# Kernel tuning notes

Hardware: AMD Instinct MI355X
Metric: run time of the kernel (lower is better)

The kernel has to match this reference:

```python
import jax, jax.numpy as jnp
import numpy as np

LAMBDA_REG = 0.1


def setup_inputs() -> dict:
    key = jax.random.key(0)
    k1, k2, k3, k4 = jax.random.split(key, 4)
    B, C, D = 4096, 10000, 128
    logits = jax.random.normal(k1, (B, C), dtype=jnp.float32)
    margins = jax.random.uniform(k2, (C,), dtype=jnp.float32)
    weights = jax.random.normal(k3, (C, D), dtype=jnp.float32)
    label = jax.random.randint(k4, (B,), 0, C, dtype=jnp.int64)
    return {"logits": logits, "margins": margins, "weights": weights, "label": label}


def reference(logits, margins, weights, label):
    B, C = logits.shape
    rows = jnp.arange(B)

    # F.cross_entropy(logits, label): mean NLL of log_softmax
    logp = jax.nn.log_softmax(logits, axis=-1)
    ce = -jnp.mean(logp[rows, label])

    # margin regularization
    margin_reg = LAMBDA_REG * jnp.mean(margins)

    # intra-class angular loss
    theta_yi = jnp.arccos(jnp.clip(logits[rows, label] / LAMBDA_REG, -1.0, 1.0))
    intra_loss = jnp.mean(theta_yi) / jnp.pi

    # inter-class loss: sum_i sum_{j != y_i} acos(clamp(w_{y_i} . w_j))
    # Vectorized replacement of the O(B*C) Python double loop:
    wy = weights[label]                       # (B, D) gather of ground-truth class rows
    S = jnp.einsum('bd,cd->bc', wy, weights)  # (B, C) pairwise dot products
    A = jnp.arccos(jnp.clip(S, -1.0, 1.0))    # (B, C) angles
    inter_sum = jnp.sum(A) - jnp.sum(A[rows, label])  # exclude j == y_i terms
    inter_loss = inter_sum / (B * (C - 1) * jnp.pi)

    return ce + margin_reg + intra_loss + inter_loss
```

## Files before the change

kernel.cpp:

```cpp
#include <hip/hip_runtime.h>
#include <stdint.h>
#include <math.h>

typedef __attribute__((ext_vector_type(8))) __bf16 bf16x8;
typedef __attribute__((ext_vector_type(4))) float floatx4;

constexpr int kB = 4096;
constexpr int kC = 10000;
constexpr int kD = 128;
constexpr int kNT = 79;
constexpr int kMT = 32;
constexpr int kBricksB = kNT * 32;
constexpr int kBricksA = kMT * 32;
constexpr int kPrepBlocks = (kBricksB + kBricksA) / 4;
constexpr float kPI = 3.14159265358979323846f;
constexpr float kLambda = 0.1f;
constexpr float kInvInter = (float)(1.0 / (4096.0 * 9999.0 * 3.141592653589793));

constexpr int kMegaBlocks = kB + kNT * kMT;
constexpr int kPerXcd = kMegaBlocks / 8;

constexpr size_t kBrickBytes = (size_t)(kBricksB + kBricksA) * 1024;
constexpr int kPartMargin = 0;
constexpr int kPartCE = 1;
constexpr int kPartInter = 1 + kB;
constexpr int kNumPart = 1 + kB + kNT * kMT;

__device__ __forceinline__ float fast_acos(float x) {
    float t = fabsf(x);
    float s = sqrtf(fmaxf(1.0f - t, 0.0f));
    float p = fmaf(fmaf(fmaf(-0.0187293f, t, 0.0742610f), t, -0.2121144f),
                   t, 1.5707288f);
    float r = s * p;
    return x < 0.0f ? kPI - r : r;
}

__device__ __forceinline__ uint16_t f2bf(float f) {
    union { float f; uint32_t u; } c; c.f = f;
    uint32_t u = c.u;
    uint32_t r = (u + 0x7FFFu + ((u >> 16) & 1u)) >> 16;
    return (uint16_t)r;
}

__global__ __launch_bounds__(256) void prep_kernel(
    const float* __restrict__ W, const float* __restrict__ margins,
    const int* __restrict__ label, uint16_t* __restrict__ wsB,
    uint16_t* __restrict__ wsA, float* __restrict__ part) {
    int blk = blockIdx.x;
    if (blk < kPrepBlocks) {
        int brick = blk * 4 + (threadIdx.x >> 6);
        int lane = threadIdx.x & 63;
        bool isA = brick >= kBricksB;
        int b2 = isA ? (brick - kBricksB) : brick;
        int kk = b2 & 3;
        int rb = (b2 >> 2) & 7;
        int tile = b2 >> 5;
        int row = tile * 128 + rb * 16 + (lane & 15);
        int k = kk * 32 + (lane >> 4) * 8;
        float v[8];
        if (isA) {
            int r = label[row];
            const float* src = W + (size_t)r * kD + k;
            #pragma unroll
            for (int j = 0; j < 8; ++j) v[j] = src[j];
        } else if (row < kC) {
            const float* src = W + (size_t)row * kD + k;
            #pragma unroll
            for (int j = 0; j < 8; ++j) v[j] = src[j];
        } else {
            #pragma unroll
            for (int j = 0; j < 8; ++j) v[j] = 0.0f;
        }
        uint4 pk;
        pk.x = (uint32_t)f2bf(v[0]) | ((uint32_t)f2bf(v[1]) << 16);
        pk.y = (uint32_t)f2bf(v[2]) | ((uint32_t)f2bf(v[3]) << 16);
        pk.z = (uint32_t)f2bf(v[4]) | ((uint32_t)f2bf(v[5]) << 16);
        pk.w = (uint32_t)f2bf(v[6]) | ((uint32_t)f2bf(v[7]) << 16);
        uint4* dst = (uint4*)(isA ? wsA : wsB);
        dst[(size_t)b2 * 64 + lane] = pk;
    } else {
        float s = 0.0f;
        for (int i = threadIdx.x; i < kC; i += 256) s += margins[i];
        for (int off = 32; off; off >>= 1) s += __shfl_down(s, off);
        __shared__ float p[4];
        if ((threadIdx.x & 63) == 0) p[threadIdx.x >> 6] = s;
        __syncthreads();
        if (threadIdx.x == 0)
            part[kPartMargin] = (p[0] + p[1] + p[2] + p[3]) * (kLambda / (float)kC);
    }
}

__global__ __launch_bounds__(256) void mega_kernel(
    const float* __restrict__ logits, const int* __restrict__ label,
    const uint16_t* __restrict__ wsA, const uint16_t* __restrict__ wsB,
    float* __restrict__ part) {
    int b = blockIdx.x;
    int x = b & 7;
    int q = b >> 3;
    int nce = (x < 6) ? 508 : 524;
    int cestart = (x < 6) ? 508 * x : 3048 + 524 * (x - 6);
    int cb = (q * nce) / kPerXcd;
    bool isce = ((q + 1) * nce) / kPerXcd > cb;
    int tid = threadIdx.x;

    if (isce) {
        int row = cestart + cb;
        const float* lp = logits + (size_t)row * kC;
        const floatx4* lp4 = (const floatx4*)lp;
        float s0 = 0.0f, s1 = 0.0f, s2 = 0.0f, s3 = 0.0f;
        floatx4 v[5];
        #pragma unroll
        for (int k = 0; k < 5; ++k)
            v[k] = __builtin_nontemporal_load(&lp4[tid + k * 256]);
        #pragma unroll
        for (int k = 0; k < 5; ++k) {
            s0 += __expf(v[k].x); s1 += __expf(v[k].y);
            s2 += __expf(v[k].z); s3 += __expf(v[k].w);
        }
        #pragma unroll
        for (int k = 0; k < 4; ++k)
            v[k] = __builtin_nontemporal_load(&lp4[tid + (5 + k) * 256]);
        #pragma unroll
        for (int k = 0; k < 4; ++k) {
            s0 += __expf(v[k].x); s1 += __expf(v[k].y);
            s2 += __expf(v[k].z); s3 += __expf(v[k].w);
        }
        if (tid < kC / 4 - 2304) {
            floatx4 vt = __builtin_nontemporal_load(&lp4[tid + 2304]);
            s0 += __expf(vt.x); s1 += __expf(vt.y);
            s2 += __expf(vt.z); s3 += __expf(vt.w);
        }
        float s = (s0 + s1) + (s2 + s3);
        for (int off = 32; off; off >>= 1) s += __shfl_down(s, off);
        __shared__ float ss[4];
        if ((tid & 63) == 0) ss[tid >> 6] = s;
        __syncthreads();
        if (tid == 0) {
            float S = (ss[0] + ss[1]) + (ss[2] + ss[3]);
            float z = lp[label[row]];
            float ce = __logf(S) - z;
            float intra =
                fast_acos(fminf(fmaxf(z * (1.0f / kLambda), -1.0f), 1.0f));
            part[kPartCE + row] = ce * (1.0f / kB) + intra * (1.0f / (kB * kPI));
        }
    } else {
        int j = q - cb;
        int mh = x & 1;
        int nq = x >> 1;
        int mt = mh * 16 + (j & 15);
        int nt = nq * 20 + (j >> 4);
        int wave = tid >> 6, lane = tid & 63;
        int wr = wave >> 1, wc = wave & 1;

        const char* gA = (const char*)wsA + (size_t)mt * 32768;
        const char* gB = (const char*)wsB + (size_t)nt * 32768;

        floatx4 zero = {0.0f, 0.0f, 0.0f, 0.0f};
        floatx4 acc[4][4];
        #pragma unroll
        for (int i = 0; i < 4; ++i)
            #pragma unroll
            for (int jj = 0; jj < 4; ++jj) acc[i][jj] = zero;

        #pragma unroll
        for (int kk = 0; kk < 4; ++kk) {
            bf16x8 a[4], bfr[4];
            #pragma unroll
            for (int i = 0; i < 4; ++i) {
                a[i] = *(const bf16x8*)(gA + ((wr * 4 + i) * 4 + kk) * 1024 +
                                        lane * 16);
                bfr[i] = *(const bf16x8*)(gB + ((wc * 4 + i) * 4 + kk) * 1024 +
                                          lane * 16);
            }
            #pragma unroll
            for (int i = 0; i < 4; ++i)
                #pragma unroll
                for (int jj = 0; jj < 4; ++jj)
                    acc[i][jj] = __builtin_amdgcn_mfma_f32_16x16x32_bf16(
                        a[i], bfr[jj], acc[i][jj], 0, 0, 0);
        }

        float local = 0.0f;
        int col0 = nt * 128 + wc * 64 + (lane & 15);
        #pragma unroll
        for (int jj = 0; jj < 4; ++jj) {
            if (col0 + jj * 16 < kC) {
                #pragma unroll
                for (int i = 0; i < 4; ++i)
                    #pragma unroll
                    for (int r = 0; r < 4; ++r)
                        local += fast_acos(
                            fminf(fmaxf(acc[i][jj][r], -1.0f), 1.0f));
            }
        }
        for (int off = 32; off; off >>= 1) local += __shfl_down(local, off);
        __shared__ float p[4];
        if (lane == 0) p[wave] = local;
        __syncthreads();
        if (tid == 0)
            part[kPartInter + mt * kNT + nt] =
                (p[0] + p[1] + p[2] + p[3]) * kInvInter;
    }
}

__global__ __launch_bounds__(256) void finalize_kernel(
    const float* __restrict__ part, float* __restrict__ out, int out_size) {
    float s = 0.0f;
    for (int i = threadIdx.x; i < kNumPart; i += 256) s += part[i];
    for (int off = 32; off; off >>= 1) s += __shfl_down(s, off);
    __shared__ float p[4];
    if ((threadIdx.x & 63) == 0) p[threadIdx.x >> 6] = s;
    __syncthreads();
    if (threadIdx.x == 0) out[0] = p[0] + p[1] + p[2] + p[3];
    for (int i = 1 + threadIdx.x; i < out_size; i += 256) out[i] = 0.0f;
}

extern "C" void kernel_launch(void* const* d_in, const int* in_sizes, int n_in,
                              void* d_out, int out_size, void* d_ws, size_t ws_size,
                              hipStream_t stream) {
    const float* logits = (const float*)d_in[0];
    const float* margins = (const float*)d_in[1];
    const float* W = (const float*)d_in[2];
    const int* label = (const int*)d_in[3];
    float* out = (float*)d_out;

    uint16_t* wsB = (uint16_t*)d_ws;
    uint16_t* wsA = (uint16_t*)((char*)d_ws + (size_t)kNT * 32768);
    float* part = (float*)((char*)d_ws + kBrickBytes);

    prep_kernel<<<kPrepBlocks + 1, 256, 0, stream>>>(W, margins, label, wsB, wsA, part);
    mega_kernel<<<kMegaBlocks, 256, 0, stream>>>(logits, label, wsA, wsB, part);
    finalize_kernel<<<1, 256, 0, stream>>>(part, out, out_size);
}
```

Baseline: 275.1 us.

## Process one CE row per wave and drop XCD-aware block interleaving

The cross-entropy branch now assigns one logits row to each wavefront, four rows per block. This removes the block-level shared-memory reduction and __syncthreads, and cuts the number of CE blocks by four. Each lane issues 13 loads in flight per batch over three batches. The XCD-aware interleave that kept GEMM tiles sharing A/B bricks on the same XCD is replaced by a simple linear interleave of CE and GEMM blocks, which may reduce L2 locality for the bf16 bricks.

```diff
diff --git a/kernel.cpp b/kernel.cpp
--- a/kernel.cpp
+++ b/kernel.cpp
@@ -17,8 +17,8 @@
 constexpr float kLambda = 0.1f;
 constexpr float kInvInter = (float)(1.0 / (4096.0 * 9999.0 * 3.141592653589793));
 
-constexpr int kMegaBlocks = kB + kNT * kMT;
-constexpr int kPerXcd = kMegaBlocks / 8;
+constexpr int kCEBlocks = kB / 4;
+constexpr int kMegaBlocks = kCEBlocks + kNT * kMT;
 
 constexpr size_t kBrickBytes = (size_t)(kBricksB + kBricksA) * 1024;
 constexpr int kPartMargin = 0;
@@ -94,62 +94,49 @@
     const float* __restrict__ logits, const int* __restrict__ label,
     const uint16_t* __restrict__ wsA, const uint16_t* __restrict__ wsB,
     float* __restrict__ part) {
+    __shared__ float red[4];
     int b = blockIdx.x;
-    int x = b & 7;
-    int q = b >> 3;
-    int nce = (x < 6) ? 508 : 524;
-    int cestart = (x < 6) ? 508 * x : 3048 + 524 * (x - 6);
-    int cb = (q * nce) / kPerXcd;
-    bool isce = ((q + 1) * nce) / kPerXcd > cb;
+    int cb = (int)(((long long)b * kCEBlocks) / kMegaBlocks);
+    bool isce = (int)(((long long)(b + 1) * kCEBlocks) / kMegaBlocks) > cb;
     int tid = threadIdx.x;
+    int wave = tid >> 6, lane = tid & 63;
 
     if (isce) {
-        int row = cestart + cb;
+        int row = cb * 4 + wave;
         const float* lp = logits + (size_t)row * kC;
         const floatx4* lp4 = (const floatx4*)lp;
+        int lbl = label[row];
+        float z = lp[lbl];
         float s0 = 0.0f, s1 = 0.0f, s2 = 0.0f, s3 = 0.0f;
-        floatx4 v[5];
-        #pragma unroll
-        for (int k = 0; k < 5; ++k)
-            v[k] = __builtin_nontemporal_load(&lp4[tid + k * 256]);
-        #pragma unroll
-        for (int k = 0; k < 5; ++k) {
-            s0 += __expf(v[k].x); s1 += __expf(v[k].y);
-            s2 += __expf(v[k].z); s3 += __expf(v[k].w);
-        }
-        #pragma unroll
-        for (int k = 0; k < 4; ++k)
-            v[k] = __builtin_nontemporal_load(&lp4[tid + (5 + k) * 256]);
-        #pragma unroll
-        for (int k = 0; k < 4; ++k) {
-            s0 += __expf(v[k].x); s1 += __expf(v[k].y);
-            s2 += __expf(v[k].z); s3 += __expf(v[k].w);
-        }
-        if (tid < kC / 4 - 2304) {
-            floatx4 vt = __builtin_nontemporal_load(&lp4[tid + 2304]);
+        floatx4 v[13];
+        #pragma unroll
+        for (int c = 0; c < 3; ++c) {
+            #pragma unroll
+            for (int k = 0; k < 13; ++k)
+                v[k] = __builtin_nontemporal_load(&lp4[lane + (c * 13 + k) * 64]);
+            #pragma unroll
+            for (int k = 0; k < 13; ++k) {
+                s0 += __expf(v[k].x); s1 += __expf(v[k].y);
+                s2 += __expf(v[k].z); s3 += __expf(v[k].w);
+            }
+        }
+        if (lane < kC / 4 - 39 * 64) {
+            floatx4 vt = __builtin_nontemporal_load(&lp4[39 * 64 + lane]);
             s0 += __expf(vt.x); s1 += __expf(vt.y);
             s2 += __expf(vt.z); s3 += __expf(vt.w);
         }
         float s = (s0 + s1) + (s2 + s3);
         for (int off = 32; off; off >>= 1) s += __shfl_down(s, off);
-        __shared__ float ss[4];
-        if ((tid & 63) == 0) ss[tid >> 6] = s;
-        __syncthreads();
-        if (tid == 0) {
-            float S = (ss[0] + ss[1]) + (ss[2] + ss[3]);
-            float z = lp[label[row]];
-            float ce = __logf(S) - z;
+        if (lane == 0) {
+            float ce = __logf(s) - z;
             float intra =
                 fast_acos(fminf(fmaxf(z * (1.0f / kLambda), -1.0f), 1.0f));
             part[kPartCE + row] = ce * (1.0f / kB) + intra * (1.0f / (kB * kPI));
         }
     } else {
-        int j = q - cb;
-        int mh = x & 1;
-        int nq = x >> 1;
-        int mt = mh * 16 + (j & 15);
-        int nt = nq * 20 + (j >> 4);
-        int wave = tid >> 6, lane = tid & 63;
+        int ii = b - cb;
+        int mt = ii / kNT;
+        int nt = ii - mt * kNT;
         int wr = wave >> 1, wc = wave & 1;
 
         const char* gA = (const char*)wsA + (size_t)mt * 32768;
@@ -194,12 +181,10 @@
             }
         }
         for (int off = 32; off; off >>= 1) local += __shfl_down(local, off);
-        __shared__ float p[4];
-        if (lane == 0) p[wave] = local;
+        if (lane == 0) red[wave] = local;
         __syncthreads();
         if (tid == 0)
-            part[kPartInter + mt * kNT + nt] =
-                (p[0] + p[1] + p[2] + p[3]) * kInvInter;
+            part[kPartInter + ii] = (red[0] + red[1] + red[2] + red[3]) * kInvInter;
     }
 }
 
```

New measurement: 276.9 us. No clear change (+0.6%).
